# Optimization experiments

Hardware: AMD Instinct MI355X
Metric: run time of the kernel (lower is better)

Reference implementation:

```python
import jax, jax.numpy as jnp
import numpy as np

WINDOW_SIZE = 11
SIGMA = 1.5
C1 = 0.01 ** 2
C2 = 0.03 ** 2


def _create_window(window_size, channel, dtype):
    coords = jnp.arange(window_size, dtype=jnp.float32) - window_size // 2
    g = jnp.exp(-coords ** 2 / (2.0 * SIGMA ** 2))
    g = g / g.sum()
    win2d = jnp.outer(g, g)  # [k, k]
    # depthwise kernel: [C, 1, k, k] in OIHW with feature_group_count=C
    return jnp.broadcast_to(win2d[None, None], (channel, 1, window_size, window_size)).astype(dtype)


def _dw_conv(x, w, channel):
    pad = WINDOW_SIZE // 2
    return jax.lax.conv_general_dilated(
        x, w,
        window_strides=(1, 1),
        padding=[(pad, pad), (pad, pad)],
        dimension_numbers=('NCHW', 'OIHW', 'NCHW'),
        feature_group_count=channel,
    )


def setup_inputs() -> dict:
    key = jax.random.key(0)
    k1, k2 = jax.random.split(key)
    shape = (16, 3, 512, 512)
    img1 = jax.random.uniform(k1, shape, dtype=jnp.float32)
    img2 = jax.random.uniform(k2, shape, dtype=jnp.float32)
    return {"img1": img1, "img2": img2}


def reference(img1, img2):
    channel = img1.shape[1]
    window = _create_window(WINDOW_SIZE, channel, img1.dtype)

    mu1 = _dw_conv(img1, window, channel)
    mu2 = _dw_conv(img2, window, channel)
    mu1_sq = mu1 * mu1
    mu2_sq = mu2 * mu2
    mu1_mu2 = mu1 * mu2

    sigma1_sq = _dw_conv(img1 * img1, window, channel) - mu1_sq
    sigma2_sq = _dw_conv(img2 * img2, window, channel) - mu2_sq
    sigma12 = _dw_conv(img1 * img2, window, channel) - mu1_mu2

    ssim_map = ((2.0 * mu1_mu2 + C1) * (2.0 * sigma12 + C2)) / (
        (mu1_sq + mu2_sq + C1) * (sigma1_sq + sigma2_sq + C2))
    # forward() returns only the mean SSIM (mcs mean is computed but discarded)
    return ssim_map.mean()
```

## Files before the change

### kernel.cpp

```cpp
#include <hip/hip_runtime.h>
#include <math.h>


#define KW 11
#define RAD 5
#define IMG_W 512
#define IMG_H 512
#define TY 23
#define NJB 3
#define NV4 70
#define C1F 0.0001f
#define C2F 0.0009f

typedef float v2f __attribute__((ext_vector_type(2)));
typedef float v4f __attribute__((ext_vector_type(4)));

__global__ __launch_bounds__(256, 3) void ssim_fused_kernel(
    const float* __restrict__ img1,
    const float* __restrict__ img2,
    float* __restrict__ out,
    float inv_n)
{
    __shared__ v4f rows[4][2][NV4];
    __shared__ float red[4];

    const int tid  = threadIdx.x;
    const int lane = tid & 63;
    const int wvi  = tid >> 6;

    const int x0 = wvi * 128;
    const int y0 = blockIdx.x * TY;

    const size_t pbase = (size_t)blockIdx.y * (size_t)(IMG_W * IMG_H);
    const float* __restrict__ p1 = img1 + pbase;
    const float* __restrict__ p2 = img2 + pbase;

    float g[KW];
    {
        double t[KW];
        double s = 0.0;
        #pragma unroll
        for (int i = 0; i < KW; ++i) {
            const double c = (double)(i - RAD);
            t[i] = exp(-(c * c) / 4.5);
            s += t[i];
        }
        #pragma unroll
        for (int i = 0; i < KW; ++i) {
            const float gi = (float)(t[i] / s);
            g[i] = __int_as_float(__builtin_amdgcn_readfirstlane(__float_as_int(gi)));
        }
    }

    const int cm  = x0 - 6 + 2 * lane;
    const int cmc = min(max(cm, 0), IMG_W - 2);
    const float mm0 = (cm     >= 0 && cm     < IMG_W) ? 1.f : 0.f;
    const float mm1 = (cm + 1 >= 0 && cm + 1 < IMG_W) ? 1.f : 0.f;
    const int ch  = x0 + 122 + 2 * lane;
    const int chc = min(max(ch, 0), IMG_W - 2);
    const float mh0 = (ch     < IMG_W) ? 1.f : 0.f;
    const float mh1 = (ch + 1 < IMG_W) ? 1.f : 0.f;

    auto load_row = [&](int j, v4f& vm, v4f& vh) {
        const int ir = y0 - RAD + j;
        vm = (v4f){0.f, 0.f, 0.f, 0.f};
        vh = (v4f){0.f, 0.f, 0.f, 0.f};
        if ((unsigned)ir < (unsigned)IMG_H) {
            const float* r1 = p1 + ir * IMG_W;
            const float* r2 = p2 + ir * IMG_W;
            const v2f a = *reinterpret_cast<const v2f*>(r1 + cmc);
            const v2f b = *reinterpret_cast<const v2f*>(r2 + cmc);
            vm = (v4f){a.x * mm0, b.x * mm0, a.y * mm1, b.y * mm1};
            if (lane < 6) {
                const v2f ah = *reinterpret_cast<const v2f*>(r1 + chc);
                const v2f bh = *reinterpret_cast<const v2f*>(r2 + chc);
                vh = (v4f){ah.x * mh0, bh.x * mh0, ah.y * mh1, bh.y * mh1};
            }
        }
    };

    v2f aMuA[KW], aSPA[KW], aMuB[KW], aSPB[KW];
    #pragma unroll
    for (int s = 0; s < KW; ++s) {
        aMuA[s] = (v2f){0.f, 0.f}; aSPA[s] = (v2f){0.f, 0.f};
        aMuB[s] = (v2f){0.f, 0.f}; aSPB[s] = (v2f){0.f, 0.f};
    }

    v4f curm, curh;
    load_row(0, curm, curh);

    float acc = 0.f;

    #pragma clang loop unroll(disable)
    for (int jb = 0; jb < NJB; ++jb) {
        #pragma unroll
        for (int P = 0; P < KW; ++P) {
            const int j   = jb * KW + P;
            const int buf = j & 1;
            v4f* __restrict__ wrow = rows[wvi][buf];

            wrow[lane] = curm;
            if (lane < 6) wrow[64 + lane] = curh;
            __threadfence_block();

            load_row(j + 1, curm, curh);

            v4f e[7];
            #pragma unroll
            for (int r = 0; r < 7; ++r) e[r] = wrow[lane + r];

            v2f hMuA = (v2f){0.f, 0.f}, hSPA = (v2f){0.f, 0.f};
            v2f hMuB = (v2f){0.f, 0.f}, hSPB = (v2f){0.f, 0.f};
            #pragma unroll
            for (int i = 1; i <= 12; ++i) {
                const v4f q = e[i >> 1];
                const v2f t = (i & 1) ? (v2f){q.z, q.w} : (v2f){q.x, q.y};
                const v2f spv = (v2f){fmaf(t.x, t.x, t.y * t.y), t.x * t.y};
                if (i <= 11) {
                    const v2f gA = (v2f){g[i - 1], g[i - 1]};
                    hMuA = __builtin_elementwise_fma(gA, t,   hMuA);
                    hSPA = __builtin_elementwise_fma(gA, spv, hSPA);
                }
                if (i >= 2) {
                    const v2f gB = (v2f){g[i - 2], g[i - 2]};
                    hMuB = __builtin_elementwise_fma(gB, t,   hMuB);
                    hSPB = __builtin_elementwise_fma(gB, spv, hSPB);
                }
            }

            #pragma unroll
            for (int s = 0; s < KW; ++s) {
                const float wt = g[(P - s + KW) % KW];
                const v2f wv2 = (v2f){wt, wt};
                if (s == P) {
                    aMuA[s] = wv2 * hMuA;  aSPA[s] = wv2 * hSPA;
                    aMuB[s] = wv2 * hMuB;  aSPB[s] = wv2 * hSPB;
                } else {
                    aMuA[s] = __builtin_elementwise_fma(wv2, hMuA, aMuA[s]);
                    aSPA[s] = __builtin_elementwise_fma(wv2, hSPA, aSPA[s]);
                    aMuB[s] = __builtin_elementwise_fma(wv2, hMuB, aMuB[s]);
                    aSPB[s] = __builtin_elementwise_fma(wv2, hSPB, aSPB[s]);
                }
            }

            const int oy = y0 + j - 2 * RAD;
            if (j >= 2 * RAD && oy < IMG_H) {
                const int e2 = (P + 1) % KW;
                #pragma unroll
                for (int px = 0; px < 2; ++px) {
                    const v2f mu = px ? aMuB[e2] : aMuA[e2];
                    const v2f SP = px ? aSPB[e2] : aSPA[e2];
                    const v2f musq = mu * mu;
                    const float mu12  = mu.x * mu.y;
                    const float musum = musq.x + musq.y;
                    const float ssum  = SP.x - musum;
                    const float s12   = SP.y - mu12;
                    const float num = fmaf(2.f, mu12, C1F) * fmaf(2.f, s12, C2F);
                    const float den = (musum + C1F) * (ssum + C2F);
                    acc = fmaf(num, __builtin_amdgcn_rcpf(den), acc);
                }
            }
        }
    }

    #pragma unroll
    for (int off = 32; off > 0; off >>= 1)
        acc += __shfl_xor(acc, off, 64);
    if (lane == 0) red[wvi] = acc;
    __syncthreads();
    if (tid == 0) {
        const float s = red[0] + red[1] + red[2] + red[3];
        atomicAdd(out, s * inv_n);
    }
}

extern "C" void kernel_launch(void* const* d_in, const int* in_sizes, int n_in,
                              void* d_out, int out_size, void* d_ws, size_t ws_size,
                              hipStream_t stream) {
    (void)in_sizes; (void)n_in; (void)d_ws; (void)ws_size;
    const float* img1 = (const float*)d_in[0];
    const float* img2 = (const float*)d_in[1];
    float* out = (float*)d_out;

    hipMemsetAsync(out, 0, (size_t)out_size * sizeof(float), stream);

    const float inv_n = 1.0f / (16.0f * 3.0f * 512.0f * 512.0f);
    dim3 grid(23, 48, 1);
    ssim_fused_kernel<<<grid, dim3(256, 1, 1), 0, stream>>>(img1, img2, out, inv_n);
}
```

Measured before the change: 169.6 us.

## Use inline packed FMA asm, symmetric Gaussian weights, and taller row tiles

Replaces compiler FMA builtins with inline v_pk_fma_f32/v_pk_mul_f32 asm and stores only six symmetric Gaussian weights as packed pairs held in VGPRs instead of scalar-broadcast floats. The first FMA of each horizontal sum becomes a multiply, removing the zero initialisation. Rows per block grow from 23 to 34 (grid 16 instead of 23), cutting halo recomputation, and the occupancy hint of 3 in launch_bounds is dropped. The result is fewer blocks (768) and possibly more register pressure, so the GPU may be less evenly filled.

```diff
diff --git a/kernel.cpp b/kernel.cpp
--- a/kernel.cpp
+++ b/kernel.cpp
@@ -6,8 +6,8 @@
 #define RAD 5
 #define IMG_W 512
 #define IMG_H 512
-#define TY 23
-#define NJB 3
+#define TY 34
+#define NJB 4
 #define NV4 70
 #define C1F 0.0001f
 #define C2F 0.0009f
@@ -15,7 +15,18 @@
 typedef float v2f __attribute__((ext_vector_type(2)));
 typedef float v4f __attribute__((ext_vector_type(4)));
 
-__global__ __launch_bounds__(256, 3) void ssim_fused_kernel(
+static __device__ __forceinline__ void pk_fma(v2f& acc, v2f a, v2f b) {
+    asm("v_pk_fma_f32 %0, %1, %2, %0" : "+v"(acc) : "v"(a), "v"(b));
+}
+static __device__ __forceinline__ v2f pk_mul(v2f a, v2f b) {
+    v2f d;
+    asm("v_pk_mul_f32 %0, %1, %2" : "=v"(d) : "v"(a), "v"(b));
+    return d;
+}
+
+#define GI(w) ((w) < 6 ? (w) : 10 - (w))
+
+__global__ __launch_bounds__(256) void ssim_fused_kernel(
     const float* __restrict__ img1,
     const float* __restrict__ img2,
     float* __restrict__ out,
@@ -35,7 +46,7 @@
     const float* __restrict__ p1 = img1 + pbase;
     const float* __restrict__ p2 = img2 + pbase;
 
-    float g[KW];
+    v2f g2[6];
     {
         double t[KW];
         double s = 0.0;
@@ -46,9 +57,9 @@
             s += t[i];
         }
         #pragma unroll
-        for (int i = 0; i < KW; ++i) {
+        for (int i = 0; i < 6; ++i) {
             const float gi = (float)(t[i] / s);
-            g[i] = __int_as_float(__builtin_amdgcn_readfirstlane(__float_as_int(gi)));
+            g2[i] = (v2f){gi, gi};
         }
     }
 
@@ -109,37 +120,33 @@
             #pragma unroll
             for (int r = 0; r < 7; ++r) e[r] = wrow[lane + r];
 
-            v2f hMuA = (v2f){0.f, 0.f}, hSPA = (v2f){0.f, 0.f};
-            v2f hMuB = (v2f){0.f, 0.f}, hSPB = (v2f){0.f, 0.f};
+            v2f hMuA, hSPA, hMuB, hSPB;
             #pragma unroll
             for (int i = 1; i <= 12; ++i) {
                 const v4f q = e[i >> 1];
                 const v2f t = (i & 1) ? (v2f){q.z, q.w} : (v2f){q.x, q.y};
                 const v2f spv = (v2f){fmaf(t.x, t.x, t.y * t.y), t.x * t.y};
                 if (i <= 11) {
-                    const v2f gA = (v2f){g[i - 1], g[i - 1]};
-                    hMuA = __builtin_elementwise_fma(gA, t,   hMuA);
-                    hSPA = __builtin_elementwise_fma(gA, spv, hSPA);
+                    const v2f gA = g2[GI(i - 1)];
+                    if (i == 1) { hMuA = pk_mul(gA, t); hSPA = pk_mul(gA, spv); }
+                    else        { pk_fma(hMuA, gA, t);  pk_fma(hSPA, gA, spv); }
                 }
                 if (i >= 2) {
-                    const v2f gB = (v2f){g[i - 2], g[i - 2]};
-                    hMuB = __builtin_elementwise_fma(gB, t,   hMuB);
-                    hSPB = __builtin_elementwise_fma(gB, spv, hSPB);
+                    const v2f gB = g2[GI(i - 2)];
+                    if (i == 2) { hMuB = pk_mul(gB, t); hSPB = pk_mul(gB, spv); }
+                    else        { pk_fma(hMuB, gB, t);  pk_fma(hSPB, gB, spv); }
                 }
             }
 
             #pragma unroll
             for (int s = 0; s < KW; ++s) {
-                const float wt = g[(P - s + KW) % KW];
-                const v2f wv2 = (v2f){wt, wt};
+                const v2f w2 = g2[GI((P - s + KW) % KW)];
                 if (s == P) {
-                    aMuA[s] = wv2 * hMuA;  aSPA[s] = wv2 * hSPA;
-                    aMuB[s] = wv2 * hMuB;  aSPB[s] = wv2 * hSPB;
+                    aMuA[s] = pk_mul(w2, hMuA);  aSPA[s] = pk_mul(w2, hSPA);
+                    aMuB[s] = pk_mul(w2, hMuB);  aSPB[s] = pk_mul(w2, hSPB);
                 } else {
-                    aMuA[s] = __builtin_elementwise_fma(wv2, hMuA, aMuA[s]);
-                    aSPA[s] = __builtin_elementwise_fma(wv2, hSPA, aSPA[s]);
-                    aMuB[s] = __builtin_elementwise_fma(wv2, hMuB, aMuB[s]);
-                    aSPB[s] = __builtin_elementwise_fma(wv2, hSPB, aSPB[s]);
+                    pk_fma(aMuA[s], w2, hMuA);   pk_fma(aSPA[s], w2, hSPA);
+                    pk_fma(aMuB[s], w2, hMuB);   pk_fma(aSPB[s], w2, hSPB);
                 }
             }
 
@@ -185,6 +192,6 @@
     hipMemsetAsync(out, 0, (size_t)out_size * sizeof(float), stream);
 
     const float inv_n = 1.0f / (16.0f * 3.0f * 512.0f * 512.0f);
-    dim3 grid(23, 48, 1);
+    dim3 grid(16, 48, 1);
     ssim_fused_kernel<<<grid, dim3(256, 1, 1), 0, stream>>>(img1, img2, out, inv_n);
 }
```

New measurement: 154.0 us. 9.2% less time.
